# Performance work log

Hardware: AMD Instinct MI355X
Metric: run time of the kernel (lower is better)

## Reference

```python
import itertools
import jax, jax.numpy as jnp
import numpy as np

B, N, D = 128, 1024, 256
G, GSZ, REL_DIM, KD, PD, NF = 64, 3, 16, 64, 64, 64


def sinusoidal_pe(n, d):
    # standard transformer sinusoidal positional encoding, shape (n, d)
    pos = jnp.arange(n, dtype=jnp.float32)[:, None]
    i = jnp.arange(d, dtype=jnp.float32)[None, :]
    angle = pos / jnp.power(10000.0, (2.0 * jnp.floor(i / 2.0)) / d)
    return jnp.where(jnp.arange(d)[None, :] % 2 == 0, jnp.sin(angle), jnp.cos(angle))


def setup_inputs() -> dict:
    key = jax.random.key(0)
    k0, k1, k2, k3, k4, k5 = jax.random.split(key, 6)
    x = jax.random.normal(k0, (B, N, D), jnp.float32)
    # graphlet filter bank (random_normal init)
    filters = 0.05 * jax.random.normal(k1, (NF, GSZ, GSZ, REL_DIM), jnp.float32)
    # learned group queries: Embedding(n_groups*graphlet_size, key_dim)
    query_emb = 0.05 * jax.random.normal(k2, (G * GSZ, KD), jnp.float32)
    # Dense(key_dim, use_bias=False) for attention keys
    Wk_map = jax.random.normal(k3, (D, KD), jnp.float32) / np.sqrt(D)
    # MultiDimInnerProdRelation: per-relation-dim query/key projections
    Wq = jax.random.normal(k4, (REL_DIM, D, PD), jnp.float32) / np.sqrt(D)
    Wk = jax.random.normal(k5, (REL_DIM, D, PD), jnp.float32) / np.sqrt(D)
    return {"x": x, "filters": filters, "query_emb": query_emb,
            "Wk_map": Wk_map, "Wq": Wq, "Wk": Wk}


def reference(x, filters, query_emb, Wk_map, Wq, Wk):
    beta = KD ** (-0.5)
    # group attention: keys = Dense(x) + positional embedding ('pos+feat')
    k = jnp.einsum('bnd,dk->bnk', x, Wk_map) + sinusoidal_pe(N, KD)[None]
    scores = jax.nn.softmax(beta * jnp.einsum('qk,bnk->bqn', query_emb, k), axis=-1)
    gobj = jnp.einsum('bqn,bnd->bqd', scores, x).reshape(B, G, GSZ, D)
    # MultiDimInnerProdRelation within each group: R[b,g,i,j,r] = <Wq_r x_i, Wk_r x_j>
    zq = jnp.einsum('bgnd,rdp->bgrnp', gobj, Wq)
    zk = jnp.einsum('bgmd,rdp->bgrmp', gobj, Wk)
    R = jnp.einsum('bgrnp,bgrmp->bgnmr', zq, zk)  # (B, G, GSZ, GSZ, REL_DIM)
    # symmetric relational inner product: aggregate (mean) over permutations
    perms = jnp.array(list(itertools.permutations(range(GSZ))))  # (P, GSZ)
    Rp = R[:, :, perms[:, :, None], perms[:, None, :], :]  # (B, G, P, GSZ, GSZ, REL_DIM)
    ip = jnp.einsum('bgpnmr,fnmr->bgpf', Rp, filters)
    return jnp.mean(ip, axis=2)  # (B, n_groups, n_filters)
```

## Files before the change

### kernel.cpp

```cpp
#include <hip/hip_runtime.h>
#include <math.h>

#define B_   128
#define N_   1024
#define D_   256
#define G_   64
#define GSZ_ 3
#define RD_  16
#define KD_  64
#define PD_  64
#define NF_  64
#define Q_   (G_*GSZ_)

typedef __attribute__((ext_vector_type(8))) short bf16x8;
typedef __attribute__((ext_vector_type(4))) float f32x4;

__device__ __forceinline__ unsigned short f2bf(float f) {
    unsigned int u = __float_as_uint(f);
    u += 0x7fffu + ((u >> 16) & 1u);
    return (unsigned short)(u >> 16);
}

__global__ void coef_kernel(const float* __restrict__ filters,
                            float* __restrict__ coef) {
    int flat = blockIdx.x * 256 + threadIdx.x;
    if (flat >= NF_ * RD_) return;
    int f = flat >> 4, r = flat & 15;
    const float* F = filters + f * 144 + r;
    float diag = F[0] + F[48 + 16] + F[96 + 32];
    float all = 0.f;
#pragma unroll
    for (int u = 0; u < 3; ++u)
#pragma unroll
        for (int v = 0; v < 3; ++v) all += F[u * 48 + v * 16];
    float a = diag * (1.f / 3.f);
    float b = (all - diag) * (1.f / 6.f);
    coef[f * 16 + r] = a - b;
    coef[1024 + f * 16 + r] = b;
}

__global__ __launch_bounds__(256)
void wb2_kernel(const float* __restrict__ Wq,
                const float* __restrict__ Wk,
                unsigned short* __restrict__ Wb) {
    __shared__ unsigned short wt[64 * 264];
    int qk = blockIdx.x >> 4, r = blockIdx.x & 15;
    const float* W = qk ? Wk : Wq;
    int t = threadIdx.x;
#pragma unroll
    for (int i = 0; i < 16; ++i) {
        int flat = i * 256 + t;
        int d = flat >> 4, p4 = flat & 15;
        float4 v = *(const float4*)(W + ((size_t)r * 256 + d) * 64 + p4 * 4);
        wt[(p4 * 4 + 0) * 264 + d] = f2bf(v.x);
        wt[(p4 * 4 + 1) * 264 + d] = f2bf(v.y);
        wt[(p4 * 4 + 2) * 264 + d] = f2bf(v.z);
        wt[(p4 * 4 + 3) * 264 + d] = f2bf(v.w);
    }
    __syncthreads();
#pragma unroll
    for (int i = 0; i < 8; ++i) {
        int flat = i * 256 + t;
        int p = flat >> 5, seg = flat & 31;
        *(uint4*)(Wb + ((size_t)(qk * 1024 + r * 64 + p)) * 256 + seg * 8) =
            *(const uint4*)(&wt[p * 264 + seg * 8]);
    }
}

__global__ void qeb_kernel(const float* __restrict__ qe,
                           unsigned short* __restrict__ qeb) {
    int i = blockIdx.x * 256 + threadIdx.x;
    if (i < Q_ * KD_) qeb[i] = f2bf(qe[i] * 0.125f);
}

__global__ void wkt_kernel(const float* __restrict__ Wk_map,
                           unsigned short* __restrict__ WkTb) {
    int i = blockIdx.x * 256 + threadIdx.x;
    int kd = i >> 8, d = i & 255;
    WkTb[kd * 256 + d] = f2bf(Wk_map[d * 64 + kd]);
}

__global__ __launch_bounds__(256)
void xt_kernel(const float* __restrict__ x,
               unsigned short* __restrict__ xTb) {
    __shared__ float xs[128][65];
    int b = blockIdx.z, d0 = blockIdx.y * 64, n0 = blockIdx.x * 128;
    int t = threadIdx.x;
#pragma unroll
    for (int i = 0; i < 8; ++i) {
        int f = i * 256 + t;
        int row = f >> 4, c4 = f & 15;
        float4 v = *(const float4*)(x + ((size_t)b * N_ + n0 + row) * D_ + d0 + c4 * 4);
        xs[row][c4 * 4 + 0] = v.x; xs[row][c4 * 4 + 1] = v.y;
        xs[row][c4 * 4 + 2] = v.z; xs[row][c4 * 4 + 3] = v.w;
    }
    __syncthreads();
#pragma unroll
    for (int i = 0; i < 4; ++i) {
        int f = i * 256 + t;
        int dr = f >> 4, seg = f & 15;
        uint4 uv;
        unsigned int* up = (unsigned int*)&uv;
#pragma unroll
        for (int j = 0; j < 4; ++j) {
            unsigned int lo = f2bf(xs[seg * 8 + 2 * j][dr]);
            unsigned int hi = f2bf(xs[seg * 8 + 2 * j + 1][dr]);
            up[j] = lo | (hi << 16);
        }
        *(uint4*)(xTb + ((size_t)b * D_ + d0 + dr) * N_ + n0 + seg * 8) = uv;
    }
}

#define WKP 264

__global__ __launch_bounds__(256, 2)
void kproj2_kernel(const float* __restrict__ x,
                   const unsigned short* __restrict__ WkTb,
                   unsigned short* __restrict__ kb) {
    __shared__ unsigned short wkts[64 * WKP];
    __shared__ unsigned short xs[64 * WKP];
    __shared__ unsigned short Ks[64 * 72];
    int b = blockIdx.y, n0 = blockIdx.x * 64;
    int t = threadIdx.x, w = t >> 6, lane = t & 63;
    int quad = lane >> 4, lcol = lane & 15;

#pragma unroll
    for (int i = 0; i < 8; ++i) {
        int f = i * 256 + t;
        int row = f >> 5, seg = f & 31;
        *(uint4*)(&wkts[row * WKP + seg * 8]) = *(const uint4*)(WkTb + row * 256 + seg * 8);
    }
#pragma unroll
    for (int i = 0; i < 16; ++i) {
        int f = i * 256 + t;
        int row = f >> 6, c4 = f & 63;
        float4 v = *(const float4*)(x + ((size_t)b * N_ + n0 + row) * D_ + c4 * 4);
        uint2 uv;
        uv.x = (unsigned int)f2bf(v.x) | ((unsigned int)f2bf(v.y) << 16);
        uv.y = (unsigned int)f2bf(v.z) | ((unsigned int)f2bf(v.w) << 16);
        *(uint2*)(&xs[row * WKP + c4 * 4]) = uv;
    }
    __syncthreads();

    f32x4 z[4];
#pragma unroll
    for (int mt = 0; mt < 4; ++mt) z[mt] = (f32x4)(0.f);
#pragma unroll
    for (int kk = 0; kk < 8; ++kk) {
        bf16x8 bf = *(const bf16x8*)(&xs[(w * 16 + lcol) * WKP + kk * 32 + quad * 8]);
#pragma unroll
        for (int mt = 0; mt < 4; ++mt) {
            bf16x8 af = *(const bf16x8*)(&wkts[(mt * 16 + lcol) * WKP + kk * 32 + quad * 8]);
            z[mt] = __builtin_amdgcn_mfma_f32_16x16x32_bf16(af, bf, z[mt], 0, 0, 0);
        }
    }

    int nl = w * 16 + lcol;
    int n = n0 + nl;
#pragma unroll
    for (int mt = 0; mt < 4; ++mt)
#pragma unroll
        for (int r = 0; r < 4; ++r) {
            int kd = mt * 16 + quad * 4 + r;
            float freq  = expf(-(float)(kd >> 1) * (logf(10000.0f) / 32.0f));
            float angle = (float)n * freq;
            float pe    = (kd & 1) ? cosf(angle) : sinf(angle);
            Ks[nl * 72 + kd] = f2bf(z[mt][r] + pe);
        }
    __syncthreads();

#pragma unroll
    for (int i = 0; i < 2; ++i) {
        int f = i * 256 + t;
        int row = f >> 3, seg = f & 7;
        *(uint4*)(kb + ((size_t)b * N_ + n0 + row) * KD_ + seg * 8) =
            *(const uint4*)(&Ks[row * 72 + seg * 8]);
    }
}

#define PSP2 136

__global__ __launch_bounds__(512, 2)
void attn4_kernel(const unsigned short* __restrict__ qeb,
                  const unsigned short* __restrict__ kb,
                  const unsigned short* __restrict__ xTb,
                  unsigned short* __restrict__ gobj) {
    __shared__ unsigned short ps[96 * PSP2];
    __shared__ float Rs[96][8];
    __shared__ float invs[96];

    int b = blockIdx.x >> 1, qh = blockIdx.x & 1;
    int t = threadIdx.x, w = t >> 6, lane = t & 63;
    int quad = lane >> 4, lcol = lane & 15;
    int q0 = qh * 96;

    bf16x8 qef[6][2];
#pragma unroll
    for (int mt = 0; mt < 6; ++mt)
#pragma unroll
        for (int ks = 0; ks < 2; ++ks)
            qef[mt][ks] = *(const bf16x8*)(qeb + (q0 + mt * 16 + lcol) * KD_ + ks * 32 + quad * 8);

    f32x4 acc[2][6];
#pragma unroll
    for (int i = 0; i < 2; ++i)
#pragma unroll
        for (int mt = 0; mt < 6; ++mt) acc[i][mt] = (f32x4)(0.f);
    float rsum[6][4];
#pragma unroll
    for (int mt = 0; mt < 6; ++mt)
#pragma unroll
        for (int r = 0; r < 4; ++r) rsum[mt][r] = 0.f;

    const unsigned short* kbB = kb + (size_t)b * N_ * KD_;
    const unsigned short* xtB = xTb + (size_t)b * D_ * N_;

    for (int c = 0; c < 8; ++c) {
        f32x4 s[6];
#pragma unroll
        for (int mt = 0; mt < 6; ++mt) s[mt] = (f32x4)(0.f);
#pragma unroll
        for (int ks = 0; ks < 2; ++ks) {
            bf16x8 bf = *(const bf16x8*)(kbB + (size_t)(c * 128 + w * 16 + lcol) * KD_ + ks * 32 + quad * 8);
#pragma unroll
            for (int mt = 0; mt < 6; ++mt)
                s[mt] = __builtin_amdgcn_mfma_f32_16x16x32_bf16(qef[mt][ks], bf, s[mt], 0, 0, 0);
        }
#pragma unroll
        for (int mt = 0; mt < 6; ++mt)
#pragma unroll
            for (int r = 0; r < 4; ++r) {
                float e = __expf(s[mt][r]);
                s[mt][r] = e;
                rsum[mt][r] += e;
            }
        __syncthreads();
#pragma unroll
        for (int mt = 0; mt < 6; ++mt)
#pragma unroll
            for (int r = 0; r < 4; ++r)
                ps[(mt * 16 + quad * 4 + r) * PSP2 + w * 16 + lcol] = f2bf(s[mt][r]);
        __syncthreads();

#pragma unroll
        for (int ks = 0; ks < 4; ++ks) {
            bf16x8 af[6];
#pragma unroll
            for (int mt = 0; mt < 6; ++mt)
                af[mt] = *(const bf16x8*)(ps + (mt * 16 + lcol) * PSP2 + ks * 32 + quad * 8);
#pragma unroll
            for (int i = 0; i < 2; ++i) {
                int dt = i * 8 + w;
                bf16x8 bf = *(const bf16x8*)(xtB + (size_t)(dt * 16 + lcol) * N_ + c * 128 + ks * 32 + quad * 8);
#pragma unroll
                for (int mt = 0; mt < 6; ++mt)
                    acc[i][mt] = __builtin_amdgcn_mfma_f32_16x16x32_bf16(af[mt], bf, acc[i][mt], 0, 0, 0);
            }
        }
    }

#pragma unroll
    for (int mt = 0; mt < 6; ++mt)
#pragma unroll
        for (int r = 0; r < 4; ++r) {
            float v = rsum[mt][r];
            v += __shfl_xor(v, 1, 64);
            v += __shfl_xor(v, 2, 64);
            v += __shfl_xor(v, 4, 64);
            v += __shfl_xor(v, 8, 64);
            rsum[mt][r] = v;
        }
    if (lcol == 0) {
#pragma unroll
        for (int mt = 0; mt < 6; ++mt)
#pragma unroll
            for (int r = 0; r < 4; ++r)
                Rs[mt * 16 + quad * 4 + r][w] = rsum[mt][r];
    }
    __syncthreads();
    if (t < 96) {
        float s8 = 0.f;
#pragma unroll
        for (int ww = 0; ww < 8; ++ww) s8 += Rs[t][ww];
        invs[t] = 1.0f / s8;
    }
    __syncthreads();

    unsigned short* gB = gobj + ((size_t)b * Q_ + q0) * D_;
#pragma unroll
    for (int i = 0; i < 2; ++i) {
        int dt = i * 8 + w;
#pragma unroll
        for (int mt = 0; mt < 6; ++mt)
#pragma unroll
            for (int r = 0; r < 4; ++r) {
                int q = mt * 16 + quad * 4 + r;
                gB[q * D_ + dt * 16 + lcol] = f2bf(acc[i][mt][r] * invs[q]);
            }
    }
}

#define AP4 264

__global__ __launch_bounds__(256, 2)
void rel4_kernel(const unsigned short* __restrict__ gobj,
                 const unsigned short* __restrict__ Wb,
                 const float* __restrict__ coef,
                 float* __restrict__ out) {
    __shared__ unsigned short As[64 * AP4];
    __shared__ float Tp[2048];

    int t = threadIdx.x, w = t >> 6, lane = t & 63;
    int quad = lane >> 4, lcol = lane & 15;
    int bg0 = blockIdx.x * 16;
    int pcol = w * 16 + lcol;

#pragma unroll
    for (int i = 0; i < 2; ++i) {
        int idx = i * 256 + t;
        int r3 = idx >> 5, c4 = idx & 31;
        uint4 zz; zz.x = zz.y = zz.z = zz.w = 0u;
        *(uint4*)(&As[(r3 * 4 + 3) * AP4 + c4 * 8]) = zz;
    }
#pragma unroll
    for (int i = 0; i < 6; ++i) {
        int idx = i * 256 + t;
        int j = idx >> 5, c4 = idx & 31;
        *(uint4*)(&As[((j / 3) * 4 + (j % 3)) * AP4 + c4 * 8]) =
            *(const uint4*)(gobj + ((size_t)(bg0 * 3 + j)) * 256 + c4 * 8);
    }
    __syncthreads();

    bf16x8 af[4][8];
#pragma unroll
    for (int mt = 0; mt < 4; ++mt)
#pragma unroll
        for (int kk = 0; kk < 8; ++kk)
            af[mt][kk] = *(const bf16x8*)(&As[(mt * 16 + lcol) * AP4 + kk * 32 + quad * 8]);

    for (int r = 0; r < 16; ++r) {
        f32x4 zq[4], zk[4];
#pragma unroll
        for (int mt = 0; mt < 4; ++mt) { zq[mt] = (f32x4)(0.f); zk[mt] = (f32x4)(0.f); }
        const unsigned short* bqp = Wb + (size_t)(r * 64 + pcol) * 256;
        const unsigned short* bkp = bqp + (size_t)1024 * 256;
#pragma unroll
        for (int kk = 0; kk < 8; ++kk) {
            int co = kk * 32 + quad * 8;
            bf16x8 bq = *(const bf16x8*)(bqp + co);
            bf16x8 bk = *(const bf16x8*)(bkp + co);
#pragma unroll
            for (int mt = 0; mt < 4; ++mt) {
                zq[mt] = __builtin_amdgcn_mfma_f32_16x16x32_bf16(af[mt][kk], bq, zq[mt], 0, 0, 0);
                zk[mt] = __builtin_amdgcn_mfma_f32_16x16x32_bf16(af[mt][kk], bk, zk[mt], 0, 0, 0);
            }
        }
#pragma unroll
        for (int mt = 0; mt < 4; ++mt) {
            float t1 = zq[mt].x * zk[mt].x + zq[mt].y * zk[mt].y +
                       zq[mt].z * zk[mt].z + zq[mt].w * zk[mt].w;
            float sq = zq[mt].x + zq[mt].y + zq[mt].z + zq[mt].w;
            float sk = zk[mt].x + zk[mt].y + zk[mt].z + zk[mt].w;
            float t2 = sq * sk;
#pragma unroll
            for (int off = 1; off < 16; off <<= 1) {
                t1 += __shfl_xor(t1, off, 64);
                t2 += __shfl_xor(t2, off, 64);
            }
            if (lcol == 0) {
                int bgl = mt * 4 + quad;
                Tp[((w * 16 + bgl) * 2 + 0) * 16 + r] = t1;
                Tp[((w * 16 + bgl) * 2 + 1) * 16 + r] = t2;
            }
        }
    }
    __syncthreads();

    int f = t & 63, grp = t >> 6;
#pragma unroll
    for (int i = 0; i < 4; ++i) {
        int bgl = grp * 4 + i;
        float a = 0.f;
#pragma unroll
        for (int r = 0; r < 16; ++r) {
            float T1 = Tp[((0 * 16 + bgl) * 2 + 0) * 16 + r] + Tp[((1 * 16 + bgl) * 2 + 0) * 16 + r] +
                       Tp[((2 * 16 + bgl) * 2 + 0) * 16 + r] + Tp[((3 * 16 + bgl) * 2 + 0) * 16 + r];
            float T2 = Tp[((0 * 16 + bgl) * 2 + 1) * 16 + r] + Tp[((1 * 16 + bgl) * 2 + 1) * 16 + r] +
                       Tp[((2 * 16 + bgl) * 2 + 1) * 16 + r] + Tp[((3 * 16 + bgl) * 2 + 1) * 16 + r];
            a += coef[f * 16 + r] * T1 + coef[1024 + f * 16 + r] * T2;
        }
        out[(size_t)(bg0 + bgl) * NF_ + f] = a;
    }
}

extern "C" void kernel_launch(void* const* d_in, const int* in_sizes, int n_in,
                              void* d_out, int out_size, void* d_ws, size_t ws_size,
                              hipStream_t stream) {
    const float* x         = (const float*)d_in[0];
    const float* filters   = (const float*)d_in[1];
    const float* query_emb = (const float*)d_in[2];
    const float* Wk_map    = (const float*)d_in[3];
    const float* Wq        = (const float*)d_in[4];
    const float* Wk        = (const float*)d_in[5];
    float* out = (float*)d_out;

    char* p = (char*)d_ws;
    unsigned short* xTb  = (unsigned short*)p;  p += (size_t)B_*D_*N_*2;
    unsigned short* kbp  = (unsigned short*)p;  p += (size_t)B_*N_*KD_*2;
    unsigned short* gobj = (unsigned short*)p;  p += (size_t)B_*Q_*D_*2;
    unsigned short* Wb   = (unsigned short*)p;  p += (size_t)2048*256*2;
    float*          coef = (float*)p;           p += 2048*4;
    unsigned short* qeb  = (unsigned short*)p;  p += (size_t)Q_*KD_*2;
    unsigned short* WkTb = (unsigned short*)p;  p += (size_t)KD_*D_*2;

    hipLaunchKernelGGL(wkt_kernel, dim3(64), dim3(256), 0, stream,
                       Wk_map, WkTb);
    hipLaunchKernelGGL(xt_kernel, dim3(8, 4, 128), dim3(256), 0, stream,
                       x, xTb);
    hipLaunchKernelGGL(kproj2_kernel, dim3(16, 128), dim3(256), 0, stream,
                       x, WkTb, kbp);
    hipLaunchKernelGGL(qeb_kernel, dim3(48), dim3(256), 0, stream,
                       query_emb, qeb);
    hipLaunchKernelGGL(coef_kernel, dim3(4), dim3(256), 0, stream,
                       filters, coef);
    hipLaunchKernelGGL(wb2_kernel, dim3(32), dim3(256), 0, stream,
                       Wq, Wk, Wb);
    hipLaunchKernelGGL(attn4_kernel, dim3(256), dim3(512), 0, stream,
                       qeb, kbp, xTb, gobj);
    hipLaunchKernelGGL(rel4_kernel, dim3(512), dim3(256), 0, stream,
                       gobj, Wb, coef, out);
}
```

Before: 358.4 us.

## Merge prep kernels and split relation kernel over relation-dim halves

Four small preprocessing kernels are fused into one prep_kernel launch, which removes several launch overheads. The relation kernel is split so each block handles half of the 16 relation dimensions, doubling the grid and combining the halves with atomicAdd into an output zeroed by memset. It also drops the register-resident A fragments in favour of per-iteration LDS reads and raises launch bounds to 4 waves per SIMD to gain occupancy. The cost is duplicated gobj staging per block, an extra memset, and atomics that make the summation order nondeterministic.

```diff
diff --git a/kernel.cpp b/kernel.cpp
--- a/kernel.cpp
+++ b/kernel.cpp
@@ -21,63 +21,63 @@
     return (unsigned short)(u >> 16);
 }
 
-__global__ void coef_kernel(const float* __restrict__ filters,
-                            float* __restrict__ coef) {
-    int flat = blockIdx.x * 256 + threadIdx.x;
-    if (flat >= NF_ * RD_) return;
-    int f = flat >> 4, r = flat & 15;
-    const float* F = filters + f * 144 + r;
-    float diag = F[0] + F[48 + 16] + F[96 + 32];
-    float all = 0.f;
-#pragma unroll
-    for (int u = 0; u < 3; ++u)
-#pragma unroll
-        for (int v = 0; v < 3; ++v) all += F[u * 48 + v * 16];
-    float a = diag * (1.f / 3.f);
-    float b = (all - diag) * (1.f / 6.f);
-    coef[f * 16 + r] = a - b;
-    coef[1024 + f * 16 + r] = b;
-}
-
 __global__ __launch_bounds__(256)
-void wb2_kernel(const float* __restrict__ Wq,
-                const float* __restrict__ Wk,
-                unsigned short* __restrict__ Wb) {
+void prep_kernel(const float* __restrict__ filters,
+                 const float* __restrict__ qe,
+                 const float* __restrict__ Wk_map,
+                 const float* __restrict__ Wq,
+                 const float* __restrict__ Wk,
+                 float* __restrict__ coef,
+                 unsigned short* __restrict__ qeb,
+                 unsigned short* __restrict__ WkTb,
+                 unsigned short* __restrict__ Wb) {
     __shared__ unsigned short wt[64 * 264];
-    int qk = blockIdx.x >> 4, r = blockIdx.x & 15;
-    const float* W = qk ? Wk : Wq;
-    int t = threadIdx.x;
-#pragma unroll
-    for (int i = 0; i < 16; ++i) {
-        int flat = i * 256 + t;
-        int d = flat >> 4, p4 = flat & 15;
-        float4 v = *(const float4*)(W + ((size_t)r * 256 + d) * 64 + p4 * 4);
-        wt[(p4 * 4 + 0) * 264 + d] = f2bf(v.x);
-        wt[(p4 * 4 + 1) * 264 + d] = f2bf(v.y);
-        wt[(p4 * 4 + 2) * 264 + d] = f2bf(v.z);
-        wt[(p4 * 4 + 3) * 264 + d] = f2bf(v.w);
-    }
-    __syncthreads();
-#pragma unroll
-    for (int i = 0; i < 8; ++i) {
-        int flat = i * 256 + t;
-        int p = flat >> 5, seg = flat & 31;
-        *(uint4*)(Wb + ((size_t)(qk * 1024 + r * 64 + p)) * 256 + seg * 8) =
-            *(const uint4*)(&wt[p * 264 + seg * 8]);
-    }
-}
-
-__global__ void qeb_kernel(const float* __restrict__ qe,
-                           unsigned short* __restrict__ qeb) {
-    int i = blockIdx.x * 256 + threadIdx.x;
-    if (i < Q_ * KD_) qeb[i] = f2bf(qe[i] * 0.125f);
-}
-
-__global__ void wkt_kernel(const float* __restrict__ Wk_map,
-                           unsigned short* __restrict__ WkTb) {
-    int i = blockIdx.x * 256 + threadIdx.x;
-    int kd = i >> 8, d = i & 255;
-    WkTb[kd * 256 + d] = f2bf(Wk_map[d * 64 + kd]);
+    int bb = blockIdx.x, t = threadIdx.x;
+    if (bb < 32) {
+        int qk = bb >> 4, r = bb & 15;
+        const float* W = qk ? Wk : Wq;
+#pragma unroll
+        for (int i = 0; i < 16; ++i) {
+            int flat = i * 256 + t;
+            int d = flat >> 4, p4 = flat & 15;
+            float4 v = *(const float4*)(W + ((size_t)r * 256 + d) * 64 + p4 * 4);
+            wt[(p4 * 4 + 0) * 264 + d] = f2bf(v.x);
+            wt[(p4 * 4 + 1) * 264 + d] = f2bf(v.y);
+            wt[(p4 * 4 + 2) * 264 + d] = f2bf(v.z);
+            wt[(p4 * 4 + 3) * 264 + d] = f2bf(v.w);
+        }
+        __syncthreads();
+#pragma unroll
+        for (int i = 0; i < 8; ++i) {
+            int flat = i * 256 + t;
+            int p = flat >> 5, seg = flat & 31;
+            *(uint4*)(Wb + ((size_t)(qk * 1024 + r * 64 + p)) * 256 + seg * 8) =
+                *(const uint4*)(&wt[p * 264 + seg * 8]);
+        }
+    } else if (bb < 96) {
+        int i = (bb - 32) * 256 + t;
+        int kd = i >> 8, d = i & 255;
+        WkTb[kd * 256 + d] = f2bf(Wk_map[d * 64 + kd]);
+    } else if (bb < 144) {
+        int i = (bb - 96) * 256 + t;
+        if (i < Q_ * KD_) qeb[i] = f2bf(qe[i] * 0.125f);
+    } else {
+        int flat = (bb - 144) * 256 + t;
+        if (flat < NF_ * RD_) {
+            int f = flat >> 4, r = flat & 15;
+            const float* F = filters + f * 144 + r;
+            float diag = F[0] + F[48 + 16] + F[96 + 32];
+            float all = 0.f;
+#pragma unroll
+            for (int u = 0; u < 3; ++u)
+#pragma unroll
+                for (int v = 0; v < 3; ++v) all += F[u * 48 + v * 16];
+            float a = diag * (1.f / 3.f);
+            float b = (all - diag) * (1.f / 6.f);
+            coef[f * 16 + r] = a - b;
+            coef[1024 + f * 16 + r] = b;
+        }
+    }
 }
 
 __global__ __launch_bounds__(256)
@@ -302,17 +302,18 @@
 
 #define AP4 264
 
-__global__ __launch_bounds__(256, 2)
-void rel4_kernel(const unsigned short* __restrict__ gobj,
+__global__ __launch_bounds__(256, 4)
+void rel5_kernel(const unsigned short* __restrict__ gobj,
                  const unsigned short* __restrict__ Wb,
                  const float* __restrict__ coef,
                  float* __restrict__ out) {
     __shared__ unsigned short As[64 * AP4];
-    __shared__ float Tp[2048];
+    __shared__ float Tp[4 * 16 * 2 * 8];
 
     int t = threadIdx.x, w = t >> 6, lane = t & 63;
     int quad = lane >> 4, lcol = lane & 15;
-    int bg0 = blockIdx.x * 16;
+    int bg0 = (blockIdx.x >> 1) * 16;
+    int rh  = blockIdx.x & 1;
     int pcol = w * 16 + lcol;
 
 #pragma unroll
@@ -331,14 +332,8 @@
     }
     __syncthreads();
 
-    bf16x8 af[4][8];
-#pragma unroll
-    for (int mt = 0; mt < 4; ++mt)
-#pragma unroll
-        for (int kk = 0; kk < 8; ++kk)
-            af[mt][kk] = *(const bf16x8*)(&As[(mt * 16 + lcol) * AP4 + kk * 32 + quad * 8]);
-
-    for (int r = 0; r < 16; ++r) {
+    for (int rr = 0; rr < 8; ++rr) {
+        int r = rh * 8 + rr;
         f32x4 zq[4], zk[4];
 #pragma unroll
         for (int mt = 0; mt < 4; ++mt) { zq[mt] = (f32x4)(0.f); zk[mt] = (f32x4)(0.f); }
@@ -351,8 +346,9 @@
             bf16x8 bk = *(const bf16x8*)(bkp + co);
 #pragma unroll
             for (int mt = 0; mt < 4; ++mt) {
-                zq[mt] = __builtin_amdgcn_mfma_f32_16x16x32_bf16(af[mt][kk], bq, zq[mt], 0, 0, 0);
-                zk[mt] = __builtin_amdgcn_mfma_f32_16x16x32_bf16(af[mt][kk], bk, zk[mt], 0, 0, 0);
+                bf16x8 af = *(const bf16x8*)(&As[(mt * 16 + lcol) * AP4 + co]);
+                zq[mt] = __builtin_amdgcn_mfma_f32_16x16x32_bf16(af, bq, zq[mt], 0, 0, 0);
+                zk[mt] = __builtin_amdgcn_mfma_f32_16x16x32_bf16(af, bk, zk[mt], 0, 0, 0);
             }
         }
 #pragma unroll
@@ -369,8 +365,8 @@
             }
             if (lcol == 0) {
                 int bgl = mt * 4 + quad;
-                Tp[((w * 16 + bgl) * 2 + 0) * 16 + r] = t1;
-                Tp[((w * 16 + bgl) * 2 + 1) * 16 + r] = t2;
+                Tp[((w * 16 + bgl) * 2 + 0) * 8 + rr] = t1;
+                Tp[((w * 16 + bgl) * 2 + 1) * 8 + rr] = t2;
             }
         }
     }
@@ -382,14 +378,15 @@
         int bgl = grp * 4 + i;
         float a = 0.f;
 #pragma unroll
-        for (int r = 0; r < 16; ++r) {
-            float T1 = Tp[((0 * 16 + bgl) * 2 + 0) * 16 + r] + Tp[((1 * 16 + bgl) * 2 + 0) * 16 + r] +
-                       Tp[((2 * 16 + bgl) * 2 + 0) * 16 + r] + Tp[((3 * 16 + bgl) * 2 + 0) * 16 + r];
-            float T2 = Tp[((0 * 16 + bgl) * 2 + 1) * 16 + r] + Tp[((1 * 16 + bgl) * 2 + 1) * 16 + r] +
-                       Tp[((2 * 16 + bgl) * 2 + 1) * 16 + r] + Tp[((3 * 16 + bgl) * 2 + 1) * 16 + r];
+        for (int rr = 0; rr < 8; ++rr) {
+            int r = rh * 8 + rr;
+            float T1 = Tp[((0 * 16 + bgl) * 2 + 0) * 8 + rr] + Tp[((1 * 16 + bgl) * 2 + 0) * 8 + rr] +
+                       Tp[((2 * 16 + bgl) * 2 + 0) * 8 + rr] + Tp[((3 * 16 + bgl) * 2 + 0) * 8 + rr];
+            float T2 = Tp[((0 * 16 + bgl) * 2 + 1) * 8 + rr] + Tp[((1 * 16 + bgl) * 2 + 1) * 8 + rr] +
+                       Tp[((2 * 16 + bgl) * 2 + 1) * 8 + rr] + Tp[((3 * 16 + bgl) * 2 + 1) * 8 + rr];
             a += coef[f * 16 + r] * T1 + coef[1024 + f * 16 + r] * T2;
         }
-        out[(size_t)(bg0 + bgl) * NF_ + f] = a;
+        atomicAdd(&out[(size_t)(bg0 + bgl) * NF_ + f], a);
     }
 }
 
@@ -413,20 +410,16 @@
     unsigned short* qeb  = (unsigned short*)p;  p += (size_t)Q_*KD_*2;
     unsigned short* WkTb = (unsigned short*)p;  p += (size_t)KD_*D_*2;
 
-    hipLaunchKernelGGL(wkt_kernel, dim3(64), dim3(256), 0, stream,
-                       Wk_map, WkTb);
+    hipMemsetAsync(out, 0, (size_t)B_ * G_ * NF_ * sizeof(float), stream);
+
+    hipLaunchKernelGGL(prep_kernel, dim3(148), dim3(256), 0, stream,
+                       filters, query_emb, Wk_map, Wq, Wk, coef, qeb, WkTb, Wb);
     hipLaunchKernelGGL(xt_kernel, dim3(8, 4, 128), dim3(256), 0, stream,
                        x, xTb);
     hipLaunchKernelGGL(kproj2_kernel, dim3(16, 128), dim3(256), 0, stream,
                        x, WkTb, kbp);
-    hipLaunchKernelGGL(qeb_kernel, dim3(48), dim3(256), 0, stream,
-                       query_emb, qeb);
-    hipLaunchKernelGGL(coef_kernel, dim3(4), dim3(256), 0, stream,
-                       filters, coef);
-    hipLaunchKernelGGL(wb2_kernel, dim3(32), dim3(256), 0, stream,
-                       Wq, Wk, Wb);
     hipLaunchKernelGGL(attn4_kernel, dim3(256), dim3(512), 0, stream,
                        qeb, kbp, xTb, gobj);
-    hipLaunchKernelGGL(rel4_kernel, dim3(512), dim3(256), 0, stream,
+    hipLaunchKernelGGL(rel5_kernel, dim3(1024), dim3(256), 0, stream,
                        gobj, Wb, coef, out);
 }
```

Result: slower. 431.5 us (+20.4%).
